# Optimization experiments

Measured on AMD Instinct MI355X. Metric: run time of the kernel, lower is better.

The kernel has to match this reference:

```python
import jax, jax.numpy as jnp
import numpy as np

NU, NB, NI, D, L = 30000, 10000, 60000, 64, 2
E_UB, E_UI, E_BI = 400000, 800000, 800000


def _graphs(rng, na, nb, ne):
    # random bipartite graph [na, nb] with ne edges; returns Laplacian-normalized
    # symmetric propagation edge list (size 2*ne over na+nb nodes) and the
    # row-normalized aggregation edge values (original MultiCBR preprocessing).
    r = rng.integers(0, na, ne).astype(np.int32)
    c = rng.integers(0, nb, ne).astype(np.int32)
    da = np.bincount(r, minlength=na).astype(np.float32)  # row degrees
    db = np.bincount(c, minlength=nb).astype(np.float32)  # col degrees
    lap = 1.0 / ((np.sqrt(da[r]) + 1e-8) * (np.sqrt(db[c]) + 1e-8))
    prop_rows = np.concatenate([r, c + na]).astype(np.int32)
    prop_cols = np.concatenate([c + na, r]).astype(np.int32)
    prop_vals = np.concatenate([lap, lap]).astype(np.float32)
    agg_vals = (1.0 / (da[r] + 1e-8)).astype(np.float32)  # diag(1/rowsum) @ G
    return prop_rows, prop_cols, prop_vals, r, c, agg_vals


def setup_inputs() -> dict:
    rng = np.random.default_rng(0)
    key = jax.random.key(0)
    ku, kb, ki = jax.random.split(key, 3)
    ub = _graphs(rng, NU, NB, E_UB)
    ui = _graphs(rng, NU, NI, E_UI)
    bi = _graphs(rng, NB, NI, E_BI)
    xav = lambda n: float(np.sqrt(2.0 / (n + D)))  # xavier_normal std
    return {
        "users_feature": jax.random.normal(ku, (NU, D), jnp.float32) * xav(NU),
        "bundles_feature": jax.random.normal(kb, (NB, D), jnp.float32) * xav(NB),
        "items_feature": jax.random.normal(ki, (NI, D), jnp.float32) * xav(NI),
        "ub_rows": jnp.asarray(ub[0]), "ub_cols": jnp.asarray(ub[1]), "ub_vals": jnp.asarray(ub[2]),
        "ui_rows": jnp.asarray(ui[0]), "ui_cols": jnp.asarray(ui[1]), "ui_vals": jnp.asarray(ui[2]),
        "bi_rows": jnp.asarray(bi[0]), "bi_cols": jnp.asarray(bi[1]), "bi_vals": jnp.asarray(bi[2]),
        "bi_agg_rows": jnp.asarray(bi[3]), "bi_agg_cols": jnp.asarray(bi[4]), "bi_agg_vals": jnp.asarray(bi[5]),
        "ui_agg_rows": jnp.asarray(ui[3]), "ui_agg_cols": jnp.asarray(ui[4]), "ui_agg_vals": jnp.asarray(ui[5]),
        "ub_layer_coefs": jnp.full((L + 1,), 1.0 / (L + 1), jnp.float32),
        "ui_layer_coefs": jnp.full((L + 1,), 1.0 / (L + 1), jnp.float32),
        "bi_layer_coefs": jnp.full((L + 1,), 1.0 / (L + 1), jnp.float32),
        "modal_coefs": jnp.asarray([0.4, 0.3, 0.3], jnp.float32),
    }


def _spmm(rows, cols, vals, feat, n):
    # sparse [n, n_src] @ feat : gather + weighted segment-sum
    return jax.ops.segment_sum(vals[:, None] * feat[cols], rows, num_segments=n)


def _l2norm(x):
    # torch F.normalize(p=2, dim=1)
    return x / jnp.maximum(jnp.linalg.norm(x, axis=1, keepdims=True), 1e-12)


def _propagate(rows, cols, vals, a, b, coefs):
    feat = jnp.concatenate([a, b], axis=0)
    n = feat.shape[0]
    acc = coefs[0] * feat  # layer-0 (un-normalized, as in original)
    for i in range(L):
        feat = _spmm(rows, cols, vals, feat, n)
        acc = acc + coefs[i + 1] * _l2norm(feat)
    return acc[: a.shape[0]], acc[a.shape[0]:]


def reference(users_feature, bundles_feature, items_feature,
              ub_rows, ub_cols, ub_vals,
              ui_rows, ui_cols, ui_vals,
              bi_rows, bi_cols, bi_vals,
              bi_agg_rows, bi_agg_cols, bi_agg_vals,
              ui_agg_rows, ui_agg_cols, ui_agg_vals,
              ub_layer_coefs, ui_layer_coefs, bi_layer_coefs, modal_coefs):
    # test=True path of get_multi_modal_representations
    ub_u, ub_b = _propagate(ub_rows, ub_cols, ub_vals, users_feature, bundles_feature, ub_layer_coefs)
    ui_u, ui_i = _propagate(ui_rows, ui_cols, ui_vals, users_feature, items_feature, ui_layer_coefs)
    bi_b, bi_i = _propagate(bi_rows, bi_cols, bi_vals, bundles_feature, items_feature, bi_layer_coefs)
    ui_b = _spmm(bi_agg_rows, bi_agg_cols, bi_agg_vals, ui_i, NB)  # BI_agg @ UI_items
    bi_u = _spmm(ui_agg_rows, ui_agg_cols, ui_agg_vals, bi_i, NU)  # UI_agg @ BI_items
    users_rep = modal_coefs[0] * ub_u + modal_coefs[1] * ui_u + modal_coefs[2] * bi_u
    bundles_rep = modal_coefs[0] * ub_b + modal_coefs[1] * ui_b + modal_coefs[2] * bi_b
    return users_rep, bundles_rep
```

## Files before the change

### kernel.cpp

```cpp
#include <hip/hip_runtime.h>

#define D 64

typedef float f2 __attribute__((ext_vector_type(2)));

__device__ __forceinline__ float blo(unsigned u) { return __uint_as_float(u << 16); }
__device__ __forceinline__ float bhi(unsigned u) { return __uint_as_float(u & 0xffff0000u); }
__device__ __forceinline__ f2 up2(unsigned u) {
    f2 r; r.x = blo(u); r.y = bhi(u); return r;
}
__device__ __forceinline__ unsigned rne(float f) {
    unsigned u = __float_as_uint(f);
    return (u + 0x7fffu + ((u >> 16) & 1u)) >> 16;
}
__device__ __forceinline__ unsigned packbf(float a, float b) {
    unsigned ub = __float_as_uint(b);
    return rne(a) | ((ub + 0x7fffu + ((ub >> 16) & 1u)) & 0xffff0000u);
}
__device__ __forceinline__ void add4(float4* p, float a, float b, float c, float d) {
    float4 o = *p; o.x += a; o.y += b; o.z += c; o.w += d; *p = o;
}

__global__ void to_bf16_kernel(const float* __restrict__ u, const float* __restrict__ b,
                               const float* __restrict__ it,
                               unsigned* __restrict__ SU, unsigned* __restrict__ SB,
                               unsigned* __restrict__ SI, int nU2, int nB2, int nI2) {
    int i = blockIdx.x * 256 + threadIdx.x;
    if (i < nU2) {
        float2 f = ((const float2*)u)[i];
        SU[i] = packbf(f.x, f.y);
    } else if (i < nU2 + nB2) {
        int j = i - nU2;
        float2 f = ((const float2*)b)[j];
        SB[j] = packbf(f.x, f.y);
    } else if (i < nU2 + nB2 + nI2) {
        int j = i - nU2 - nB2;
        float2 f = ((const float2*)it)[j];
        SI[j] = packbf(f.x, f.y);
    }
}


__global__ void hist_kernel(const int* __restrict__ r0, const int* __restrict__ r1,
                            const int* __restrict__ r2,
                            int ne0, int ne1, int ne2, int n0, int n1, int n2,
                            int* __restrict__ histG) {
    __shared__ int h[512];
    int t = threadIdx.x;
    int g = blockIdx.x >> 8, blk = blockIdx.x & 255;
    const int* rows = (g == 0) ? r0 : (g == 1) ? r1 : r2;
    int ne = (g == 0) ? ne0 : (g == 1) ? ne1 : ne2;
    unsigned n = (unsigned)((g == 0) ? n0 : (g == 1) ? n1 : n2);
    h[t] = 0; h[t + 256] = 0;
    __syncthreads();
    int C = (ne + 255) >> 8;
    int e0 = blk * C, e1 = min(ne, e0 + C);
    for (int e = e0 + t; e < e1; e += 256) {
        unsigned b = ((unsigned)rows[e] << 9) / n;
        atomicAdd(&h[b], 1);
    }
    __syncthreads();
    histG[(((g << 9) | t) << 8) | blk] = h[t];
    histG[(((g << 9) | (t + 256)) << 8) | blk] = h[t + 256];
}

__global__ void scan1_kernel(const int* __restrict__ deg, int* __restrict__ rs,
                             int* __restrict__ bsum, int n) {
    __shared__ int tmp[256];
    int t = threadIdx.x;
    int g = blockIdx.x * 256 + t;
    int v = (g < n) ? deg[g] : 0;
    tmp[t] = v;
    __syncthreads();
    for (int off = 1; off < 256; off <<= 1) {
        int x = (t >= off) ? tmp[t - off] : 0;
        __syncthreads();
        tmp[t] += x;
        __syncthreads();
    }
    if (g < n) rs[g] = tmp[t] - v;
    if (t == 255) bsum[blockIdx.x] = tmp[255];
}

__global__ void scan2_kernel(int* __restrict__ bsum, int B) {
    __shared__ int tmp[2048];
    int t = threadIdx.x;
    int v0 = (t < B) ? bsum[t] : 0;
    int v1 = (t + 1024 < B) ? bsum[t + 1024] : 0;
    tmp[t] = v0; tmp[t + 1024] = v1;
    __syncthreads();
    for (int off = 1; off < 2048; off <<= 1) {
        int a0 = (t >= off) ? tmp[t - off] : 0;
        int a1 = ((t + 1024) >= off) ? tmp[t + 1024 - off] : 0;
        __syncthreads();
        tmp[t] += a0; tmp[t + 1024] += a1;
        __syncthreads();
    }
    if (t < B) bsum[t] = tmp[t] - v0;
    if (t + 1024 < B) bsum[t + 1024] = tmp[t + 1024] - v1;
}

__global__ void scan3_kernel(int* __restrict__ rs, const int* __restrict__ bsum, int n) {
    int g = blockIdx.x * blockDim.x + threadIdx.x;
    if (g < n) rs[g] += bsum[g >> 8];
}

__global__ void bucket_scatter_kernel(const int* __restrict__ r0, const int* __restrict__ c0,
                                      const int* __restrict__ r1, const int* __restrict__ c1,
                                      const int* __restrict__ r2, const int* __restrict__ c2,
                                      int ne0, int ne1, int ne2, int n0, int n1, int n2,
                                      const int* __restrict__ hofs, unsigned* __restrict__ ebuf) {
    __shared__ int cur[512];
    int t = threadIdx.x;
    int g = blockIdx.x >> 8, blk = blockIdx.x & 255;
    const int* rows = (g == 0) ? r0 : (g == 1) ? r1 : r2;
    const int* cols = (g == 0) ? c0 : (g == 1) ? c1 : c2;
    int ne = (g == 0) ? ne0 : (g == 1) ? ne1 : ne2;
    int n  = (g == 0) ? n0  : (g == 1) ? n1  : n2;
    cur[t] = hofs[(((g << 9) | t) << 8) | blk];
    cur[t + 256] = hofs[(((g << 9) | (t + 256)) << 8) | blk];
    __syncthreads();
    int C = (ne + 255) >> 8;
    int e0 = blk * C, e1 = min(ne, e0 + C);
    for (int e = e0 + t; e < e1; e += 256) {
        int r = rows[e];
        unsigned b = ((unsigned)r << 9) / (unsigned)n;
        int rb0 = ((int)b * n + 511) >> 9;
        int pos = atomicAdd(&cur[b], 1);
        ebuf[pos] = ((unsigned)(r - rb0) << 23) | (unsigned)cols[e];
    }
}

__global__ void sort_bucket_kernel(const unsigned* __restrict__ ebuf, const int* __restrict__ hofs,
                                   int* __restrict__ rs0, int* __restrict__ rs1, int* __restrict__ rs2,
                                   float* __restrict__ isd0, float* __restrict__ isd1,
                                   float* __restrict__ isd2, int* __restrict__ ccol,
                                   int ne0, int ne1, int ne2, int n0, int n1, int n2) {
    __shared__ int cnt[256];
    __shared__ int pfx[256];
    int t = threadIdx.x;
    int g = blockIdx.x >> 9, b = blockIdx.x & 511;
    int ne = (g == 0) ? ne0 : (g == 1) ? ne1 : ne2;
    int n  = (g == 0) ? n0  : (g == 1) ? n1  : n2;
    int O  = (g == 0) ? 0   : (g == 1) ? ne0 : ne0 + ne1;
    int*   rs  = (g == 0) ? rs0  : (g == 1) ? rs1  : rs2;
    float* isd = (g == 0) ? isd0 : (g == 1) ? isd1 : isd2;
    int rb0 = (b * n + 511) >> 9;
    int rb1 = ((b + 1) * n + 511) >> 9;
    int R = rb1 - rb0;
    cnt[t] = 0;
    __syncthreads();
    int base = hofs[((g << 9) | b) << 8];
    int end  = (b == 511) ? (O + ne) : hofs[((g << 9) | (b + 1)) << 8];
    for (int e = base + t; e < end; e += 256)
        atomicAdd(&cnt[ebuf[e] >> 23], 1);
    __syncthreads();
    pfx[t] = cnt[t];
    __syncthreads();
    for (int off = 1; off < 256; off <<= 1) {
        int v = (t >= off) ? pfx[t - off] : 0;
        __syncthreads();
        pfx[t] += v;
        __syncthreads();
    }
    int c0 = cnt[t], ex = pfx[t] - c0;
    if (t < R) {
        rs[rb0 + t] = base + ex - O;
        isd[rb0 + t] = 1.0f / (sqrtf((float)c0) + 1e-8f);
    }
    __syncthreads();
    cnt[t] = base + ex;
    __syncthreads();
    for (int e = base + t; e < end; e += 256) {
        unsigned p = ebuf[e];
        int pos = atomicAdd(&cnt[p >> 23], 1);
        ccol[pos] = (int)(p & 0x7fffffu);
    }
    if (b == 511 && t == 0) rs[n] = ne;
}

struct GA {
    const int* rs; const int* ccol; const float* isd;
    const unsigned* srcA; const unsigned* srcB; int na;
    const float* inA; const float* inB;
    unsigned* feat_out; float* dst0; void* dst1;
    const float* coefs; const float* modalp; int mi; int n;
};

template <bool FIRST, bool A0, bool A1, bool BF16D1>
__global__ void spmm_norm_kernel(GA A, GA B, int ntot) {
    int row = blockIdx.x * (blockDim.x >> 6) + (threadIdx.x >> 6);
    if (row >= ntot) return;
    GA G; int r;
    if (row < A.n) { G = A; r = row; }
    else           { G = B; r = row - A.n; if (r >= G.n) return; }
    int lane = threadIdx.x & 63;
    int g = lane >> 3, q = lane & 7;
    int s = G.rs[r], e = G.rs[r + 1];
    float isr = G.isd[r];
    const unsigned* src; int coff;
    if (FIRST && r < G.na) { src = G.srcB; coff = G.na; }
    else                   { src = G.srcA; coff = 0; }
    src += (q << 2);
    const int* cc = G.ccol;
    const float* isdp = G.isd;
    f2 acc2[4];
#pragma unroll
    for (int j = 0; j < 4; ++j) acc2[j] = (f2){0.f, 0.f};
    int k = s + g;
    if (FIRST) {
        for (; k + 8 < e; k += 16) {
            int c0 = cc[k], c1 = cc[k + 8];
            float v0 = isdp[c0], v1 = isdp[c1];
            uint4 f0 = *(const uint4*)(src + (size_t)(c0 - coff) * 32);
            uint4 f1 = *(const uint4*)(src + (size_t)(c1 - coff) * 32);
            f2 v02 = {v0, v0}, v12 = {v1, v1};
            acc2[0] = v02 * up2(f0.x) + acc2[0];
            acc2[1] = v02 * up2(f0.y) + acc2[1];
            acc2[2] = v02 * up2(f0.z) + acc2[2];
            acc2[3] = v02 * up2(f0.w) + acc2[3];
            acc2[0] = v12 * up2(f1.x) + acc2[0];
            acc2[1] = v12 * up2(f1.y) + acc2[1];
            acc2[2] = v12 * up2(f1.z) + acc2[2];
            acc2[3] = v12 * up2(f1.w) + acc2[3];
        }
        if (k < e) {
            int c0 = cc[k];
            float v0 = isdp[c0];
            uint4 f0 = *(const uint4*)(src + (size_t)(c0 - coff) * 32);
            f2 v02 = {v0, v0};
            acc2[0] = v02 * up2(f0.x) + acc2[0];
            acc2[1] = v02 * up2(f0.y) + acc2[1];
            acc2[2] = v02 * up2(f0.z) + acc2[2];
            acc2[3] = v02 * up2(f0.w) + acc2[3];
        }
    } else {
        for (; k + 8 < e; k += 16) {
            int c0 = cc[k], c1 = cc[k + 8];
            uint4 f0 = *(const uint4*)(src + (size_t)c0 * 32);
            uint4 f1 = *(const uint4*)(src + (size_t)c1 * 32);
            acc2[0] += up2(f0.x); acc2[1] += up2(f0.y);
            acc2[2] += up2(f0.z); acc2[3] += up2(f0.w);
            acc2[0] += up2(f1.x); acc2[1] += up2(f1.y);
            acc2[2] += up2(f1.z); acc2[3] += up2(f1.w);
        }
        if (k < e) {
            int c0 = cc[k];
            uint4 f0 = *(const uint4*)(src + (size_t)c0 * 32);
            acc2[0] += up2(f0.x); acc2[1] += up2(f0.y);
            acc2[2] += up2(f0.z); acc2[3] += up2(f0.w);
        }
    }
    float a[8] = {acc2[0].x, acc2[0].y, acc2[1].x, acc2[1].y,
                  acc2[2].x, acc2[2].y, acc2[3].x, acc2[3].y};
#pragma unroll
    for (int o = 8; o < 64; o <<= 1) {
#pragma unroll
        for (int j = 0; j < 8; ++j) a[j] += __shfl_xor(a[j], o, 64);
    }
    float s2 = 0.f;
#pragma unroll
    for (int j = 0; j < 8; ++j) s2 += a[j] * a[j];
#pragma unroll
    for (int o = 1; o < 8; o <<= 1) s2 += __shfl_xor(s2, o, 64);
    if (g != 0) return;
    float inv = 1.0f / fmaxf(sqrtf(s2), 1e-12f);
    float mm = G.modalp[G.mi];
    size_t ro = (size_t)r * D + (q << 3);
    float ctb[8];
    if (FIRST) {
        float isr2 = isr * isr;
        uint4 fw;
        fw.x = packbf(isr2 * a[0], isr2 * a[1]);
        fw.y = packbf(isr2 * a[2], isr2 * a[3]);
        fw.z = packbf(isr2 * a[4], isr2 * a[5]);
        fw.w = packbf(isr2 * a[6], isr2 * a[7]);
        *(uint4*)(G.feat_out + (size_t)r * 32 + (q << 2)) = fw;
        const float* ib = (r < G.na) ? (G.inA + ro) : (G.inB + (size_t)(r - G.na) * D + (q << 3));
        float4 a0 = *(const float4*)ib;
        float4 a1 = *(const float4*)(ib + 4);
        float c0 = G.coefs[0], c1m = G.coefs[1] * inv;
        ctb[0] = mm * fmaf(c0, a0.x, c1m * a[0]);
        ctb[1] = mm * fmaf(c0, a0.y, c1m * a[1]);
        ctb[2] = mm * fmaf(c0, a0.z, c1m * a[2]);
        ctb[3] = mm * fmaf(c0, a0.w, c1m * a[3]);
        ctb[4] = mm * fmaf(c0, a1.x, c1m * a[4]);
        ctb[5] = mm * fmaf(c0, a1.y, c1m * a[5]);
        ctb[6] = mm * fmaf(c0, a1.z, c1m * a[6]);
        ctb[7] = mm * fmaf(c0, a1.w, c1m * a[7]);
    } else {
        float mc = mm * G.coefs[2] * inv;
#pragma unroll
        for (int j = 0; j < 8; ++j) ctb[j] = mc * a[j];
    }
    if (r < G.na) {
        if (A0) {
            *(float4*)(G.dst0 + ro) = make_float4(ctb[0], ctb[1], ctb[2], ctb[3]);
            *(float4*)(G.dst0 + ro + 4) = make_float4(ctb[4], ctb[5], ctb[6], ctb[7]);
        } else {
            add4((float4*)(G.dst0 + ro), ctb[0], ctb[1], ctb[2], ctb[3]);
            add4((float4*)(G.dst0 + ro + 4), ctb[4], ctb[5], ctb[6], ctb[7]);
        }
    } else if (BF16D1) {
        unsigned* p = (unsigned*)G.dst1 + (size_t)(r - G.na) * 32 + (q << 2);
        if (!A1) {
            uint4 cur = *(const uint4*)p;
            ctb[0] += blo(cur.x); ctb[1] += bhi(cur.x);
            ctb[2] += blo(cur.y); ctb[3] += bhi(cur.y);
            ctb[4] += blo(cur.z); ctb[5] += bhi(cur.z);
            ctb[6] += blo(cur.w); ctb[7] += bhi(cur.w);
        }
        uint4 w;
        w.x = packbf(ctb[0], ctb[1]); w.y = packbf(ctb[2], ctb[3]);
        w.z = packbf(ctb[4], ctb[5]); w.w = packbf(ctb[6], ctb[7]);
        *(uint4*)p = w;
    } else {
        float* d1 = (float*)G.dst1 + (size_t)(r - G.na) * D + (q << 3);
        add4((float4*)d1, ctb[0], ctb[1], ctb[2], ctb[3]);
        add4((float4*)(d1 + 4), ctb[4], ctb[5], ctb[6], ctb[7]);
    }
}

__global__ void agg2_kernel(const int* __restrict__ rsA, const int* __restrict__ ccA,
                            const unsigned* __restrict__ sA, float* __restrict__ oA,
                            int naA, int nA,
                            const int* __restrict__ rsB, const int* __restrict__ ccB,
                            const unsigned* __restrict__ sB, float* __restrict__ oB,
                            int naB, int nB) {
    int row = blockIdx.x * (blockDim.x >> 6) + (threadIdx.x >> 6);
    if (row >= nA + nB) return;
    const int* rs; const int* cc; const unsigned* src; float* out; int na; int r;
    if (row < nA) { rs = rsA; cc = ccA; src = sA; out = oA; na = naA; r = row; }
    else          { rs = rsB; cc = ccB; src = sB; out = oB; na = naB; r = row - nA; }
    int lane = threadIdx.x & 63;
    int g = lane >> 3, q = lane & 7;
    src += (q << 2);
    int s = rs[r], e = rs[r + 1];
    f2 acc2[4];
#pragma unroll
    for (int j = 0; j < 4; ++j) acc2[j] = (f2){0.f, 0.f};
    int k = s + g;
    for (; k + 8 < e; k += 16) {
        int c0 = cc[k] - na, c1 = cc[k + 8] - na;
        uint4 f0 = *(const uint4*)(src + (size_t)c0 * 32);
        uint4 f1 = *(const uint4*)(src + (size_t)c1 * 32);
        acc2[0] += up2(f0.x); acc2[1] += up2(f0.y);
        acc2[2] += up2(f0.z); acc2[3] += up2(f0.w);
        acc2[0] += up2(f1.x); acc2[1] += up2(f1.y);
        acc2[2] += up2(f1.z); acc2[3] += up2(f1.w);
    }
    if (k < e) {
        int c0 = cc[k] - na;
        uint4 f0 = *(const uint4*)(src + (size_t)c0 * 32);
        acc2[0] += up2(f0.x); acc2[1] += up2(f0.y);
        acc2[2] += up2(f0.z); acc2[3] += up2(f0.w);
    }
    float a[8] = {acc2[0].x, acc2[0].y, acc2[1].x, acc2[1].y,
                  acc2[2].x, acc2[2].y, acc2[3].x, acc2[3].y};
#pragma unroll
    for (int o = 8; o < 64; o <<= 1) {
#pragma unroll
        for (int j = 0; j < 8; ++j) a[j] += __shfl_xor(a[j], o, 64);
    }
    if (g != 0) return;
    float ad = 1.0f / ((float)(e - s) + 1e-8f);
    float* p = out + (size_t)r * D + (q << 3);
    add4((float4*)p, ad * a[0], ad * a[1], ad * a[2], ad * a[3]);
    add4((float4*)(p + 4), ad * a[4], ad * a[5], ad * a[6], ad * a[7]);
}

extern "C" void kernel_launch(void* const* d_in, const int* in_sizes, int n_in,
                              void* d_out, int out_size, void* d_ws, size_t ws_size,
                              hipStream_t stream) {
    const float* users   = (const float*)d_in[0];
    const float* bundles = (const float*)d_in[1];
    const float* items   = (const float*)d_in[2];
    const int*   ub_rows = (const int*)d_in[3];
    const int*   ub_cols = (const int*)d_in[4];
    const int*   ui_rows = (const int*)d_in[6];
    const int*   ui_cols = (const int*)d_in[7];
    const int*   bi_rows = (const int*)d_in[9];
    const int*   bi_cols = (const int*)d_in[10];
    const float* ub_coefs = (const float*)d_in[18];
    const float* ui_coefs = (const float*)d_in[19];
    const float* bi_coefs = (const float*)d_in[20];
    const float* modal    = (const float*)d_in[21];

    const int NU_ = in_sizes[0] / D;
    const int NB_ = in_sizes[1] / D;
    const int NI_ = in_sizes[2] / D;
    const int ne_ub = in_sizes[3];
    const int ne_ui = in_sizes[6];
    const int ne_bi = in_sizes[9];

    const int n_ui = NU_ + NI_;
    const int n_bi = NB_ + NI_;
    const int n_ub = NU_ + NB_;

    float* out = (float*)d_out;

    int*      rs_ui  = (int*)d_ws;
    int*      rs_bi  = rs_ui + 90112;
    int*      rs_ub  = rs_bi + 70144;
    float*    isd_ui = (float*)(rs_ub + 40192);
    float*    isd_bi = isd_ui + 90112;
    float*    isd_ub = isd_bi + 70144;
    int*      hofs   = (int*)(isd_ub + 40192);
    int*      bsum   = hofs + 393280;
    int*      ccol   = bsum + 2048;
    int*      histG  = ccol;
    unsigned* SU     = (unsigned*)(ccol + 4000000);
    unsigned* SB     = SU + 960000;
    unsigned* SI     = SB + 320000;
    unsigned* ovl    = SI + 1920000;
    unsigned* ebuf   = ovl;
    unsigned* sfB_ui = ovl;
    unsigned* sfB_bi = sfB_ui + 2880000;
    unsigned* IT1b   = sfB_bi + 2240000;
    unsigned* IT2b   = IT1b + 1920000;
    unsigned* sfB_ub = IT1b;

    int* ccol_ui = ccol;
    int* ccol_bi = ccol + ne_ui;
    int* ccol_ub = ccol + ne_ui + ne_bi;

    float* out_u = out;
    float* out_b = out + (size_t)NU_ * D;

    {
        int tot2 = (NU_ + NB_ + NI_) * 32;
        to_bf16_kernel<<<(tot2 + 255) / 256, 256, 0, stream>>>(
            users, bundles, items, SU, SB, SI, NU_ * 32, NB_ * 32, NI_ * 32);
    }

    hist_kernel<<<768, 256, 0, stream>>>(ui_rows, bi_rows, ub_rows,
                                         ne_ui, ne_bi, ne_ub, n_ui, n_bi, n_ub, histG);
    scan1_kernel<<<1536, 256, 0, stream>>>(histG, hofs, bsum, 393216);
    scan2_kernel<<<1, 1024, 0, stream>>>(bsum, 1536);
    scan3_kernel<<<1536, 256, 0, stream>>>(hofs, bsum, 393216);
    bucket_scatter_kernel<<<768, 256, 0, stream>>>(
        ui_rows, ui_cols, bi_rows, bi_cols, ub_rows, ub_cols,
        ne_ui, ne_bi, ne_ub, n_ui, n_bi, n_ub, hofs, ebuf);
    sort_bucket_kernel<<<1536, 256, 0, stream>>>(
        ebuf, hofs, rs_ui, rs_bi, rs_ub, isd_ui, isd_bi, isd_ub, ccol,
        ne_ui, ne_bi, ne_ub, n_ui, n_bi, n_ub);

    GA gUI = { rs_ui, ccol_ui, isd_ui, SU, SI, NU_, users, items,
               sfB_ui, out_u, (void*)IT1b, ui_coefs, modal, 1, n_ui };
    GA gBI = { rs_bi, ccol_bi, isd_bi, SB, SI, NB_, bundles, items,
               sfB_bi, out_b, (void*)IT2b, bi_coefs, modal, 2, n_bi };
    GA gUB = { rs_ub, ccol_ub, isd_ub, SU, SB, NU_, users, bundles,
               sfB_ub, out_u, (void*)out_b, ub_coefs, modal, 0, n_ub };
    GA gUI2 = gUI; gUI2.srcA = sfB_ui;
    GA gBI2 = gBI; gBI2.srcA = sfB_bi;
    GA gUB2 = gUB; gUB2.srcA = sfB_ub;

    int ntotL = n_ui + n_bi;
    spmm_norm_kernel<true,  true,  true,  true ><<<(ntotL + 3) / 4, 256, 0, stream>>>(gUI,  gBI,  ntotL);
    spmm_norm_kernel<false, false, false, true ><<<(ntotL + 3) / 4, 256, 0, stream>>>(gUI2, gBI2, ntotL);

    agg2_kernel<<<(NU_ + NB_ + 3) / 4, 256, 0, stream>>>(
        rs_ui, ccol_ui, IT2b, out_u, NU_, NU_,
        rs_bi, ccol_bi, IT1b, out_b, NB_, NB_);

    spmm_norm_kernel<true,  false, false, false><<<(n_ub + 3) / 4, 256, 0, stream>>>(gUB,  gUB,  n_ub);
    spmm_norm_kernel<false, false, false, false><<<(n_ub + 3) / 4, 256, 0, stream>>>(gUB2, gUB2, n_ub);
}
```

Measured before the change: 509.0 us.

## Map one row per 8-lane group instead of one row per wavefront in SpMM

The SpMM and aggregation kernels now give each row to an 8-lane group, so a wavefront handles 8 rows instead of splitting one row's edges across 8 groups. This removes the cross-group shuffle reduction and the idle lanes in the epilogue, and launches 8x fewer blocks. The cost is less parallelism per row: each group walks its whole edge list serially, and divergence grows when row degrees within a wavefront differ. Early exits now happen per group, so the remaining shuffles run with some lanes inactive, which may be fragile.

```diff
diff --git a/kernel.cpp b/kernel.cpp
--- a/kernel.cpp
+++ b/kernel.cpp
@@ -1,14 +1,9 @@
 #include <hip/hip_runtime.h>
 
 #define D 64
-
-typedef float f2 __attribute__((ext_vector_type(2)));
 
 __device__ __forceinline__ float blo(unsigned u) { return __uint_as_float(u << 16); }
 __device__ __forceinline__ float bhi(unsigned u) { return __uint_as_float(u & 0xffff0000u); }
-__device__ __forceinline__ f2 up2(unsigned u) {
-    f2 r; r.x = blo(u); r.y = bhi(u); return r;
-}
 __device__ __forceinline__ unsigned rne(float f) {
     unsigned u = __float_as_uint(f);
     return (u + 0x7fffu + ((u >> 16) & 1u)) >> 16;
@@ -39,7 +34,6 @@
         SI[j] = packbf(f.x, f.y);
     }
 }
-
 
 __global__ void hist_kernel(const int* __restrict__ r0, const int* __restrict__ r1,
                             const int* __restrict__ r2,
@@ -189,13 +183,13 @@
 
 template <bool FIRST, bool A0, bool A1, bool BF16D1>
 __global__ void spmm_norm_kernel(GA A, GA B, int ntot) {
-    int row = blockIdx.x * (blockDim.x >> 6) + (threadIdx.x >> 6);
+    int lane = threadIdx.x & 63;
+    int row = (blockIdx.x * (blockDim.x >> 6) + (threadIdx.x >> 6)) * 8 + (lane >> 3);
     if (row >= ntot) return;
     GA G; int r;
     if (row < A.n) { G = A; r = row; }
     else           { G = B; r = row - A.n; if (r >= G.n) return; }
-    int lane = threadIdx.x & 63;
-    int g = lane >> 3, q = lane & 7;
+    int q = lane & 7;
     int s = G.rs[r], e = G.rs[r + 1];
     float isr = G.isd[r];
     const unsigned* src; int coff;
@@ -204,66 +198,53 @@
     src += (q << 2);
     const int* cc = G.ccol;
     const float* isdp = G.isd;
-    f2 acc2[4];
+    float a[8];
 #pragma unroll
-    for (int j = 0; j < 4; ++j) acc2[j] = (f2){0.f, 0.f};
-    int k = s + g;
-    if (FIRST) {
-        for (; k + 8 < e; k += 16) {
-            int c0 = cc[k], c1 = cc[k + 8];
+    for (int j = 0; j < 8; ++j) a[j] = 0.f;
+    int k = s;
+    for (; k + 1 < e; k += 2) {
+        int c0 = cc[k], c1 = cc[k + 1];
+        uint4 f0 = *(const uint4*)(src + (size_t)(c0 - coff) * 32);
+        uint4 f1 = *(const uint4*)(src + (size_t)(c1 - coff) * 32);
+        if (FIRST) {
             float v0 = isdp[c0], v1 = isdp[c1];
-            uint4 f0 = *(const uint4*)(src + (size_t)(c0 - coff) * 32);
-            uint4 f1 = *(const uint4*)(src + (size_t)(c1 - coff) * 32);
-            f2 v02 = {v0, v0}, v12 = {v1, v1};
-            acc2[0] = v02 * up2(f0.x) + acc2[0];
-            acc2[1] = v02 * up2(f0.y) + acc2[1];
-            acc2[2] = v02 * up2(f0.z) + acc2[2];
-            acc2[3] = v02 * up2(f0.w) + acc2[3];
-            acc2[0] = v12 * up2(f1.x) + acc2[0];
-            acc2[1] = v12 * up2(f1.y) + acc2[1];
-            acc2[2] = v12 * up2(f1.z) + acc2[2];
-            acc2[3] = v12 * up2(f1.w) + acc2[3];
+            a[0] = fmaf(v0, blo(f0.x), a[0]); a[1] = fmaf(v0, bhi(f0.x), a[1]);
+            a[2] = fmaf(v0, blo(f0.y), a[2]); a[3] = fmaf(v0, bhi(f0.y), a[3]);
+            a[4] = fmaf(v0, blo(f0.z), a[4]); a[5] = fmaf(v0, bhi(f0.z), a[5]);
+            a[6] = fmaf(v0, blo(f0.w), a[6]); a[7] = fmaf(v0, bhi(f0.w), a[7]);
+            a[0] = fmaf(v1, blo(f1.x), a[0]); a[1] = fmaf(v1, bhi(f1.x), a[1]);
+            a[2] = fmaf(v1, blo(f1.y), a[2]); a[3] = fmaf(v1, bhi(f1.y), a[3]);
+            a[4] = fmaf(v1, blo(f1.z), a[4]); a[5] = fmaf(v1, bhi(f1.z), a[5]);
+            a[6] = fmaf(v1, blo(f1.w), a[6]); a[7] = fmaf(v1, bhi(f1.w), a[7]);
+        } else {
+            a[0] += blo(f0.x) + blo(f1.x); a[1] += bhi(f0.x) + bhi(f1.x);
+            a[2] += blo(f0.y) + blo(f1.y); a[3] += bhi(f0.y) + bhi(f1.y);
+            a[4] += blo(f0.z) + blo(f1.z); a[5] += bhi(f0.z) + bhi(f1.z);
+            a[6] += blo(f0.w) + blo(f1.w); a[7] += bhi(f0.w) + bhi(f1.w);
         }
-        if (k < e) {
-            int c0 = cc[k];
+    }
+    if (k < e) {
+        int c0 = cc[k];
+        uint4 f0 = *(const uint4*)(src + (size_t)(c0 - coff) * 32);
+        if (FIRST) {
             float v0 = isdp[c0];
-            uint4 f0 = *(const uint4*)(src + (size_t)(c0 - coff) * 32);
-            f2 v02 = {v0, v0};
-            acc2[0] = v02 * up2(f0.x) + acc2[0];
-            acc2[1] = v02 * up2(f0.y) + acc2[1];
-            acc2[2] = v02 * up2(f0.z) + acc2[2];
-            acc2[3] = v02 * up2(f0.w) + acc2[3];
+            a[0] = fmaf(v0, blo(f0.x), a[0]); a[1] = fmaf(v0, bhi(f0.x), a[1]);
+            a[2] = fmaf(v0, blo(f0.y), a[2]); a[3] = fmaf(v0, bhi(f0.y), a[3]);
+            a[4] = fmaf(v0, blo(f0.z), a[4]); a[5] = fmaf(v0, bhi(f0.z), a[5]);
+            a[6] = fmaf(v0, blo(f0.w), a[6]); a[7] = fmaf(v0, bhi(f0.w), a[7]);
+        } else {
+            a[0] += blo(f0.x); a[1] += bhi(f0.x);
+            a[2] += blo(f0.y); a[3] += bhi(f0.y);
+            a[4] += blo(f0.z); a[5] += bhi(f0.z);
+            a[6] += blo(f0.w); a[7] += bhi(f0.w);
         }
-    } else {
-        for (; k + 8 < e; k += 16) {
-            int c0 = cc[k], c1 = cc[k + 8];
-            uint4 f0 = *(const uint4*)(src + (size_t)c0 * 32);
-            uint4 f1 = *(const uint4*)(src + (size_t)c1 * 32);
-            acc2[0] += up2(f0.x); acc2[1] += up2(f0.y);
-            acc2[2] += up2(f0.z); acc2[3] += up2(f0.w);
-            acc2[0] += up2(f1.x); acc2[1] += up2(f1.y);
-            acc2[2] += up2(f1.z); acc2[3] += up2(f1.w);
-        }
-        if (k < e) {
-            int c0 = cc[k];
-            uint4 f0 = *(const uint4*)(src + (size_t)c0 * 32);
-            acc2[0] += up2(f0.x); acc2[1] += up2(f0.y);
-            acc2[2] += up2(f0.z); acc2[3] += up2(f0.w);
-        }
-    }
-    float a[8] = {acc2[0].x, acc2[0].y, acc2[1].x, acc2[1].y,
-                  acc2[2].x, acc2[2].y, acc2[3].x, acc2[3].y};
-#pragma unroll
-    for (int o = 8; o < 64; o <<= 1) {
-#pragma unroll
-        for (int j = 0; j < 8; ++j) a[j] += __shfl_xor(a[j], o, 64);
     }
     float s2 = 0.f;
 #pragma unroll
     for (int j = 0; j < 8; ++j) s2 += a[j] * a[j];
-#pragma unroll
-    for (int o = 1; o < 8; o <<= 1) s2 += __shfl_xor(s2, o, 64);
-    if (g != 0) return;
+    s2 += __shfl_xor(s2, 1, 64);
+    s2 += __shfl_xor(s2, 2, 64);
+    s2 += __shfl_xor(s2, 4, 64);
     float inv = 1.0f / fmaxf(sqrtf(s2), 1e-12f);
     float mm = G.modalp[G.mi];
     size_t ro = (size_t)r * D + (q << 3);
@@ -327,42 +308,36 @@
                             const int* __restrict__ rsB, const int* __restrict__ ccB,
                             const unsigned* __restrict__ sB, float* __restrict__ oB,
                             int naB, int nB) {
-    int row = blockIdx.x * (blockDim.x >> 6) + (threadIdx.x >> 6);
+    int lane = threadIdx.x & 63;
+    int row = (blockIdx.x * (blockDim.x >> 6) + (threadIdx.x >> 6)) * 8 + (lane >> 3);
     if (row >= nA + nB) return;
     const int* rs; const int* cc; const unsigned* src; float* out; int na; int r;
     if (row < nA) { rs = rsA; cc = ccA; src = sA; out = oA; na = naA; r = row; }
     else          { rs = rsB; cc = ccB; src = sB; out = oB; na = naB; r = row - nA; }
-    int lane = threadIdx.x & 63;
-    int g = lane >> 3, q = lane & 7;
+    int q = lane & 7;
     src += (q << 2);
     int s = rs[r], e = rs[r + 1];
-    f2 acc2[4];
+    float a[8];
 #pragma unroll
-    for (int j = 0; j < 4; ++j) acc2[j] = (f2){0.f, 0.f};
-    int k = s + g;
-    for (; k + 8 < e; k += 16) {
-        int c0 = cc[k] - na, c1 = cc[k + 8] - na;
+    for (int j = 0; j < 8; ++j) a[j] = 0.f;
+    int k = s;
+    for (; k + 1 < e; k += 2) {
+        int c0 = cc[k] - na, c1 = cc[k + 1] - na;
         uint4 f0 = *(const uint4*)(src + (size_t)c0 * 32);
         uint4 f1 = *(const uint4*)(src + (size_t)c1 * 32);
-        acc2[0] += up2(f0.x); acc2[1] += up2(f0.y);
-        acc2[2] += up2(f0.z); acc2[3] += up2(f0.w);
-        acc2[0] += up2(f1.x); acc2[1] += up2(f1.y);
-        acc2[2] += up2(f1.z); acc2[3] += up2(f1.w);
+        a[0] += blo(f0.x) + blo(f1.x); a[1] += bhi(f0.x) + bhi(f1.x);
+        a[2] += blo(f0.y) + blo(f1.y); a[3] += bhi(f0.y) + bhi(f1.y);
+        a[4] += blo(f0.z) + blo(f1.z); a[5] += bhi(f0.z) + bhi(f1.z);
+        a[6] += blo(f0.w) + blo(f1.w); a[7] += bhi(f0.w) + bhi(f1.w);
     }
     if (k < e) {
         int c0 = cc[k] - na;
         uint4 f0 = *(const uint4*)(src + (size_t)c0 * 32);
-        acc2[0] += up2(f0.x); acc2[1] += up2(f0.y);
-        acc2[2] += up2(f0.z); acc2[3] += up2(f0.w);
-    }
-    float a[8] = {acc2[0].x, acc2[0].y, acc2[1].x, acc2[1].y,
-                  acc2[2].x, acc2[2].y, acc2[3].x, acc2[3].y};
-#pragma unroll
-    for (int o = 8; o < 64; o <<= 1) {
-#pragma unroll
-        for (int j = 0; j < 8; ++j) a[j] += __shfl_xor(a[j], o, 64);
-    }
-    if (g != 0) return;
+        a[0] += blo(f0.x); a[1] += bhi(f0.x);
+        a[2] += blo(f0.y); a[3] += bhi(f0.y);
+        a[4] += blo(f0.z); a[5] += bhi(f0.z);
+        a[6] += blo(f0.w); a[7] += bhi(f0.w);
+    }
     float ad = 1.0f / ((float)(e - s) + 1e-8f);
     float* p = out + (size_t)r * D + (q << 3);
     add4((float4*)p, ad * a[0], ad * a[1], ad * a[2], ad * a[3]);
@@ -456,13 +431,13 @@
     GA gUB2 = gUB; gUB2.srcA = sfB_ub;
 
     int ntotL = n_ui + n_bi;
-    spmm_norm_kernel<true,  true,  true,  true ><<<(ntotL + 3) / 4, 256, 0, stream>>>(gUI,  gBI,  ntotL);
-    spmm_norm_kernel<false, false, false, true ><<<(ntotL + 3) / 4, 256, 0, stream>>>(gUI2, gBI2, ntotL);
-
-    agg2_kernel<<<(NU_ + NB_ + 3) / 4, 256, 0, stream>>>(
+    spmm_norm_kernel<true,  true,  true,  true ><<<(ntotL + 31) / 32, 256, 0, stream>>>(gUI,  gBI,  ntotL);
+    spmm_norm_kernel<false, false, false, true ><<<(ntotL + 31) / 32, 256, 0, stream>>>(gUI2, gBI2, ntotL);
+
+    agg2_kernel<<<(NU_ + NB_ + 31) / 32, 256, 0, stream>>>(
         rs_ui, ccol_ui, IT2b, out_u, NU_, NU_,
         rs_bi, ccol_bi, IT1b, out_b, NB_, NB_);
 
-    spmm_norm_kernel<true,  false, false, false><<<(n_ub + 3) / 4, 256, 0, stream>>>(gUB,  gUB,  n_ub);
-    spmm_norm_kernel<false, false, false, false><<<(n_ub + 3) / 4, 256, 0, stream>>>(gUB2, gUB2, n_ub);
-}
+    spmm_norm_kernel<true,  false, false, false><<<(n_ub + 31) / 32, 256, 0, stream>>>(gUB,  gUB,  n_ub);
+    spmm_norm_kernel<false, false, false, false><<<(n_ub + 31) / 32, 256, 0, stream>>>(gUB2, gUB2, n_ub);
+}
```

Result: faster. 495.2 us (-2.7%).
